# Kernel optimization log

Hardware: AMD Instinct MI355X
Metric: run time of the kernel (lower is better)

## Reference

```python
import jax, jax.numpy as jnp
import numpy as np

K = 16  # neighborhood size, fixed by the module

def knn_idx(coor_k, coor_q, k=K):
    # coor_*: [B, 3, N]; returns idx [B, k, Nq] into the Nk axis (transpose_mode=False layout)
    q = coor_q.transpose(0, 2, 1)
    r = coor_k.transpose(0, 2, 1)
    d2 = (jnp.sum(q * q, -1)[:, :, None] + jnp.sum(r * r, -1)[:, None, :]
          - 2.0 * jnp.einsum('bqd,bnd->bqn', q, r))
    _, idx = jax.lax.top_k(-d2, k)  # [B, Nq, k], nearest first
    return idx.transpose(0, 2, 1)   # [B, k, Nq]

def get_graph_feature(coor_q, x_q, coor_k, x_k, k=K):
    # Faithful to the source, including the flat gather + reshape(B, Nq, k, C)
    # applied to a [B, k, Nq]-ordered index (the source does NOT transpose idx).
    B, C, Nq = x_q.shape
    Nk = x_k.shape[2]
    idx = jax.lax.stop_gradient(knn_idx(coor_k, coor_q, k))            # [B, k, Nq]
    idx_flat = (idx + jnp.arange(B)[:, None, None] * Nk).reshape(-1)
    xk_flat = x_k.transpose(0, 2, 1).reshape(-1, C)                     # [B*Nk, C]
    feat = xk_flat[idx_flat].reshape(B, Nq, k, C).transpose(0, 3, 1, 2)  # [B, C, Nq, k]
    xq = jnp.broadcast_to(x_q[:, :, :, None], (B, C, Nq, k))
    return jnp.concatenate([feat - xq, xq], axis=1)                     # [B, 2C, Nq, k]

def group_norm(x, gamma, beta, groups=4, eps=1e-5):
    B, C, N, Kk = x.shape
    xg = x.reshape(B, groups, C // groups, N, Kk)
    mu = jnp.mean(xg, axis=(2, 3, 4), keepdims=True)
    var = jnp.var(xg, axis=(2, 3, 4), keepdims=True)
    xn = ((xg - mu) * jax.lax.rsqrt(var + eps)).reshape(B, C, N, Kk)
    return xn * gamma[None, :, None, None] + beta[None, :, None, None]

def edge_layer(h, w, gamma, beta):
    # Conv2d 1x1 (no bias) + GroupNorm(4) + LeakyReLU(0.2)
    return jax.nn.leaky_relu(group_norm(jnp.einsum('bcnk,oc->bonk', h, w), gamma, beta), 0.2)

def fps(xyz, m):
    # furthest point sampling, pointnet2 semantics (start at index 0). xyz: [B, N, 3]
    B, N, _ = xyz.shape
    def body(i, state):
        dists, far, idxs = state
        idxs = idxs.at[:, i].set(far)
        centroid = jnp.take_along_axis(xyz, far[:, None, None], axis=1)  # [B,1,3]
        d = jnp.sum((xyz - centroid) ** 2, axis=-1)
        dists = jnp.minimum(dists, d)
        return (dists, jnp.argmax(dists, axis=-1).astype(jnp.int32), idxs)
    state = (jnp.full((B, N), 1e10, xyz.dtype), jnp.zeros((B,), jnp.int32),
             jnp.zeros((B, m), jnp.int32))
    return jax.lax.fori_loop(0, m, body, state)[2]

def fps_downsample(coor, x, m):
    idx = fps(jax.lax.stop_gradient(coor).transpose(0, 2, 1), m)  # [B, m]
    comb = jnp.concatenate([coor, x], axis=1)                      # [B, 3+C, N]
    new = jnp.take_along_axis(comb, idx[:, None, :], axis=2)       # [B, 3+C, m]
    return new[:, :3], new[:, 3:]

def setup_inputs():
    key = jax.random.key(0)
    ks = jax.random.split(key, 16)
    B, N = 8, 2048
    p = lambda k, s, sc=0.05: jax.random.normal(k, s, jnp.float32) * sc
    return {
        'x': jax.random.normal(ks[0], (B, 3, N), jnp.float32),
        'w_in': p(ks[1], (8, 3)), 'b_in': p(ks[2], (8,)),
        'w1': p(ks[3], (32, 16)), 'g1': 1.0 + p(ks[4], (32,)), 'be1': p(ks[5], (32,)),
        'w2': p(ks[6], (64, 64)), 'g2': 1.0 + p(ks[7], (64,)), 'be2': p(ks[8], (64,)),
        'w3': p(ks[9], (64, 128)), 'g3': 1.0 + p(ks[10], (64,)), 'be3': p(ks[11], (64,)),
        'w4': p(ks[12], (128, 128)), 'g4': 1.0 + p(ks[13], (128,)), 'be4': p(ks[14], (128,)),
    }

def reference(x, w_in, b_in, w1, g1, be1, w2, g2, be2, w3, g3, be3, w4, g4, be4):
    N = x.shape[2]
    coor = x
    f = jnp.einsum('bcn,oc->bon', x, w_in) + b_in[None, :, None]          # input_trans Conv1d
    f = jnp.max(edge_layer(get_graph_feature(coor, f, coor, f), w1, g1, be1), axis=-1)
    coor_q, f_q = fps_downsample(coor, f, N // 4)
    f = jnp.max(edge_layer(get_graph_feature(coor_q, f_q, coor, f), w2, g2, be2), axis=-1)
    coor = coor_q
    f = jnp.max(edge_layer(get_graph_feature(coor, f, coor, f), w3, g3, be3), axis=-1)
    coor_q, f_q = fps_downsample(coor, f, N // 16)
    f = jnp.max(edge_layer(get_graph_feature(coor_q, f_q, coor, f), w4, g4, be4), axis=-1)
    return (coor_q, f)  # [B,3,N//16], [B,128,N//16]
```

## Files before the change

kernel.cpp:

```cpp
#include <hip/hip_runtime.h>
#include <float.h>
#include <stdint.h>


#define DI __device__ __forceinline__
DI float f_add(float a, float b) { return __fadd_rn(a, b); }
DI float f_sub(float a, float b) { return __fsub_rn(a, b); }
DI float f_mul(float a, float b) { return __fmul_rn(a, b); }

DI uint64_t umax64(uint64_t a, uint64_t b) { return a > b ? a : b; }

template<int CTRL, int RMASK>
DI uint32_t dpp_umax32(uint32_t v) {
  uint32_t o = (uint32_t)__builtin_amdgcn_update_dpp(0, (int)v, CTRL, RMASK, 0xF, false);
  return v > o ? v : o;
}
template<int CTRL, int RMASK>
DI uint32_t dpp_umin32(uint32_t v) {
  uint32_t o = (uint32_t)__builtin_amdgcn_update_dpp(-1, (int)v, CTRL, RMASK, 0xF, false);
  return v < o ? v : o;
}
template<int CTRL, int RMASK>
DI float dpp_fmin32(float v) {
  int o = __builtin_amdgcn_update_dpp(0x7F7FFFFF , __float_as_int(v),
                                      CTRL, RMASK, 0xF, false);
  return fminf(v, __int_as_float(o));
}
DI uint32_t wave_umax_bcast32(uint32_t v) {
  v = dpp_umax32<0x111, 0xF>(v);
  v = dpp_umax32<0x112, 0xF>(v);
  v = dpp_umax32<0x114, 0xF>(v);
  v = dpp_umax32<0x118, 0xF>(v);
  v = dpp_umax32<0x142, 0xA>(v);
  v = dpp_umax32<0x143, 0xC>(v);
  return (uint32_t)__builtin_amdgcn_readlane((int)v, 63);
}
DI uint32_t wave_umin_bcast32(uint32_t v) {
  v = dpp_umin32<0x111, 0xF>(v);
  v = dpp_umin32<0x112, 0xF>(v);
  v = dpp_umin32<0x114, 0xF>(v);
  v = dpp_umin32<0x118, 0xF>(v);
  v = dpp_umin32<0x142, 0xA>(v);
  v = dpp_umin32<0x143, 0xC>(v);
  return (uint32_t)__builtin_amdgcn_readlane((int)v, 63);
}
DI float wave_fmin_bcast32(float v) {
  v = dpp_fmin32<0x111, 0xF>(v);
  v = dpp_fmin32<0x112, 0xF>(v);
  v = dpp_fmin32<0x114, 0xF>(v);
  v = dpp_fmin32<0x118, 0xF>(v);
  v = dpp_fmin32<0x142, 0xA>(v);
  v = dpp_fmin32<0x143, 0xC>(v);
  return __int_as_float(__builtin_amdgcn_readlane(__float_as_int(v), 63));
}

template<int NK>
DI void knn_body(const float* __restrict__ cq, int Nq,
                 const float* __restrict__ ck, int* __restrict__ out,
                 int b, int qbase, float* smem)
{
  constexpr int CPL = NK / 64;
  float* xs = smem;
  float* ys = smem + NK;
  float* zs = smem + 2*NK;
  float* rr = smem + 3*NK;
  const int tid = threadIdx.x;
  for (int i = tid; i < NK; i += 256) {
    float a  = ck[((size_t)b*3 + 0)*NK + i];
    float bb = ck[((size_t)b*3 + 1)*NK + i];
    float c  = ck[((size_t)b*3 + 2)*NK + i];
    xs[i] = a; ys[i] = bb; zs[i] = c;
    rr[i] = f_add(f_add(f_mul(a,a), f_mul(bb,bb)), f_mul(c,c));
  }
  __syncthreads();
  const int lane = tid & 63, w = tid >> 6;
  const int q = qbase + w;
  if (q >= Nq) return;
  float qx = cq[((size_t)b*3 + 0)*Nq + q];
  float qy = cq[((size_t)b*3 + 1)*Nq + q];
  float qz = cq[((size_t)b*3 + 2)*Nq + q];
  float qq = f_add(f_add(f_mul(qx,qx), f_mul(qy,qy)), f_mul(qz,qz));
  float v[CPL];
  #pragma unroll
  for (int j = 0; j < CPL; ++j) {
    int c = j*64 + lane;
    float dot = f_add(f_add(f_mul(qx,xs[c]), f_mul(qy,ys[c])), f_mul(qz,zs[c]));
    v[j] = f_sub(f_add(qq, rr[c]), f_mul(2.0f, dot));
  }
  unsigned mask = (CPL >= 32) ? 0xFFFFFFFFu : ((1u << CPL) - 1u);
  for (int r = 0; r < 16; ++r) {
    float bv = FLT_MAX; int bc = 0x7FFFFFFF;
    #pragma unroll
    for (int j = 0; j < CPL; ++j) {
      float vj = ((mask >> j) & 1u) ? v[j] : FLT_MAX;
      if (vj < bv) { bv = vj; bc = j*64 + lane; }
    }
    float wmin = wave_fmin_bcast32(bv);
    uint32_t cand = (bv == wmin) ? (uint32_t)bc : 0xFFFFFFFFu;
    uint32_t wbc = wave_umin_bcast32(cand);
    if ((wbc & 63) == (uint32_t)lane) mask &= ~(1u << (wbc >> 6));
    if (lane == 0) out[((size_t)b*16 + r)*Nq + q] = (int)wbc;
  }
}

__device__ void fps_body(const float* __restrict__ x, int b,
                         int* __restrict__ s1, float* __restrict__ coorq,
                         int* __restrict__ s2, float* __restrict__ coorq2,
                         float* __restrict__ outc, char* smem_raw)
{
  float4*   pts  = (float4*)smem_raw;
  int*      sel  = (int*)(smem_raw + 32768);
  uint64_t* wkey = (uint64_t*)(smem_raw + 32768 + 2048);
  const int tid = threadIdx.x, lane = tid & 63, w = tid >> 6;

  for (int i = tid; i < 2048; i += 256)
    pts[i] = make_float4(x[((size_t)b*3 + 0)*2048 + i],
                         x[((size_t)b*3 + 1)*2048 + i],
                         x[((size_t)b*3 + 2)*2048 + i], 0.f);
  __syncthreads();

  float px[8], py[8], pz[8], dl[8];
  #pragma unroll
  for (int j = 0; j < 8; ++j) {
    float4 p = pts[tid + 256*j];
    px[j] = p.x; py[j] = p.y; pz[j] = p.z; dl[j] = 1e10f;
  }

  int far = 0;
  float4 c = pts[0];
  for (int i = 0; i < 512; ++i) {
    if (tid == 0) sel[i] = far;
    float bd = -1.0f; uint32_t bi = 0;
    #pragma unroll
    for (int j = 0; j < 8; ++j) {
      float dx = f_sub(px[j], c.x);
      float dy = f_sub(py[j], c.y);
      float dz = f_sub(pz[j], c.z);
      float d  = f_add(f_add(f_mul(dx,dx), f_mul(dy,dy)), f_mul(dz,dz));
      float nd = fminf(dl[j], d);
      dl[j] = nd;
      if (nd > bd) { bd = nd; bi = (uint32_t)(tid + 256*j); }
    }
    uint32_t db = __float_as_uint(bd);
    uint32_t wd = wave_umax_bcast32(db);
    uint32_t cand = (db == wd) ? bi : 0xFFFFFFFFu;
    uint32_t wi = wave_umin_bcast32(cand);
    if (lane == 0) wkey[(i & 1)*4 + w] = ((uint64_t)wd << 32) | (uint32_t)~wi;
    __syncthreads();
    const uint64_t* wk = wkey + (i & 1)*4;
    uint64_t g = umax64(umax64(wk[0], wk[1]), umax64(wk[2], wk[3]));
    far = (int)~(uint32_t)g;
    c = pts[far];
  }
  __syncthreads();

  int p0 = sel[tid], p1 = sel[tid + 256];
  float4 v0 = pts[p0], v1 = pts[p1];
  s1[b*512 + tid]       = p0;
  s1[b*512 + tid + 256] = p1;
  coorq[((size_t)b*3 + 0)*512 + tid] = v0.x;
  coorq[((size_t)b*3 + 1)*512 + tid] = v0.y;
  coorq[((size_t)b*3 + 2)*512 + tid] = v0.z;
  coorq[((size_t)b*3 + 0)*512 + tid + 256] = v1.x;
  coorq[((size_t)b*3 + 1)*512 + tid + 256] = v1.y;
  coorq[((size_t)b*3 + 2)*512 + tid + 256] = v1.z;
  __syncthreads();
  pts[tid] = v0; pts[tid + 256] = v1;
  __syncthreads();

  if (w == 0) {
    float qx[8], qy[8], qz[8], d2[8];
    #pragma unroll
    for (int j = 0; j < 8; ++j) {
      float4 p = pts[lane + 64*j];
      qx[j] = p.x; qy[j] = p.y; qz[j] = p.z; d2[j] = 1e10f;
    }
    int far2 = 0;
    float cx = pts[0].x, cy = pts[0].y, cz = pts[0].z;
    for (int i = 0; i < 128; ++i) {
      if (lane == 0) sel[i] = far2;
      float bd = -1.0f; uint32_t bi = 0;
      #pragma unroll
      for (int j = 0; j < 8; ++j) {
        float dx = f_sub(qx[j], cx);
        float dy = f_sub(qy[j], cy);
        float dz = f_sub(qz[j], cz);
        float d  = f_add(f_add(f_mul(dx,dx), f_mul(dy,dy)), f_mul(dz,dz));
        float nd = fminf(d2[j], d);
        d2[j] = nd;
        if (nd > bd) { bd = nd; bi = (uint32_t)(lane + 64*j); }
      }
      uint32_t db = __float_as_uint(bd);
      uint32_t wd = wave_umax_bcast32(db);
      uint32_t cand = (db == wd) ? bi : 0xFFFFFFFFu;
      uint32_t wi = wave_umin_bcast32(cand);
      far2 = (int)wi;
      uint32_t js = wi >> 6, ls = wi & 63;
      float sx = qx[0], sy = qy[0], sz = qz[0];
      #pragma unroll
      for (uint32_t t = 1; t < 8; ++t) {
        sx = (js == t) ? qx[t] : sx;
        sy = (js == t) ? qy[t] : sy;
        sz = (js == t) ? qz[t] : sz;
      }
      cx = __int_as_float(__builtin_amdgcn_readlane(__float_as_int(sx), ls));
      cy = __int_as_float(__builtin_amdgcn_readlane(__float_as_int(sy), ls));
      cz = __int_as_float(__builtin_amdgcn_readlane(__float_as_int(sz), ls));
    }
  }
  __syncthreads();
  if (tid < 128) {
    int p = sel[tid];
    float4 v = pts[p];
    s2[b*128 + tid] = p;
    coorq2[((size_t)b*3 + 0)*128 + tid] = v.x;
    coorq2[((size_t)b*3 + 1)*128 + tid] = v.y;
    coorq2[((size_t)b*3 + 2)*128 + tid] = v.z;
    outc[((size_t)b*3 + 0)*128 + tid] = v.x;
    outc[((size_t)b*3 + 1)*128 + tid] = v.y;
    outc[((size_t)b*3 + 2)*128 + tid] = v.z;
  }
}

__device__ void fused_l1_body(const float* __restrict__ x,
                              const float* __restrict__ w_in, const float* __restrict__ b_in,
                              const float* __restrict__ w1,
                              float* __restrict__ ymax1, float* __restrict__ ymin1,
                              float* __restrict__ stats,
                              int b, int S, char* smem_raw)
{
  float* xs = (float*)smem_raw;
  float* ys = xs + 2048;
  float* zs = xs + 4096;
  float* rr = xs + 6144;
  int*   idxloc = (int*)(xs + 8192);
  float* sw1  = (float*)(idxloc + 256);
  float* winb = sw1 + 512;
  float* red  = winb + 32;
  const int tid = threadIdx.x, lane = tid & 63, w = tid >> 6;

  for (int i = tid; i < 2048; i += 256) {
    float a  = x[((size_t)b*3 + 0)*2048 + i];
    float bb = x[((size_t)b*3 + 1)*2048 + i];
    float c  = x[((size_t)b*3 + 2)*2048 + i];
    xs[i] = a; ys[i] = bb; zs[i] = c;
    rr[i] = f_add(f_add(f_mul(a,a), f_mul(bb,bb)), f_mul(c,c));
  }
  for (int i = tid; i < 512; i += 256) sw1[i] = w1[i];
  if (tid < 24) winb[tid] = w_in[tid];
  if (tid < 8)  winb[24 + tid] = b_in[tid];
  __syncthreads();

  for (int qq = 0; qq < 4; ++qq) {
    int qi = w*4 + qq;
    int q = S + qi;
    float qx = xs[q], qy = ys[q], qz = zs[q];
    float qqv = f_add(f_add(f_mul(qx,qx), f_mul(qy,qy)), f_mul(qz,qz));
    float v[32];
    #pragma unroll
    for (int j = 0; j < 32; ++j) {
      int c = j*64 + lane;
      float dot = f_add(f_add(f_mul(qx,xs[c]), f_mul(qy,ys[c])), f_mul(qz,zs[c]));
      v[j] = f_sub(f_add(qqv, rr[c]), f_mul(2.0f, dot));
    }
    unsigned mask = 0xFFFFFFFFu;
    for (int r = 0; r < 16; ++r) {
      float bv = FLT_MAX; int bc = 0x7FFFFFFF;
      #pragma unroll
      for (int j = 0; j < 32; ++j) {
        float vj = ((mask >> j) & 1u) ? v[j] : FLT_MAX;
        if (vj < bv) { bv = vj; bc = j*64 + lane; }
      }
      float wmin = wave_fmin_bcast32(bv);
      uint32_t cand = (bv == wmin) ? (uint32_t)bc : 0xFFFFFFFFu;
      uint32_t wbc = wave_umin_bcast32(cand);
      if ((wbc & 63) == (uint32_t)lane) mask &= ~(1u << (wbc >> 6));
      if (lane == 0) idxloc[qi*16 + r] = (int)wbc;
    }
  }
  __syncthreads();

  const int r = tid >> 4, k = tid & 15;
  const int nbr = idxloc[k*16 + r];
  const int ng  = r*128 + (S >> 4);
  float f0n[8], f0q[8], h[8];
  #pragma unroll
  for (int o = 0; o < 8; ++o) {
    f0n[o] = winb[o*3+0]*xs[nbr] + winb[o*3+1]*ys[nbr] + winb[o*3+2]*zs[nbr] + winb[24+o];
    f0q[o] = winb[o*3+0]*xs[ng]  + winb[o*3+1]*ys[ng]  + winb[o*3+2]*zs[ng]  + winb[24+o];
    h[o] = f0n[o] - f0q[o];
  }
  float gsum[4] = {0.f,0.f,0.f,0.f}, gsq[4] = {0.f,0.f,0.f,0.f};
  float* ymx = ymax1 + ((size_t)b*2048 + ng)*32;
  float* ymn = ymin1 + ((size_t)b*2048 + ng)*32;
  for (int o = 0; o < 32; ++o) {
    const float4* wr = (const float4*)(sw1 + o*16);
    float4 wa = wr[0], wb4 = wr[1], wc = wr[2], wd = wr[3];
    float acc = wa.x*h[0]+wa.y*h[1]+wa.z*h[2]+wa.w*h[3]
              + wb4.x*h[4]+wb4.y*h[5]+wb4.z*h[6]+wb4.w*h[7]
              + wc.x*f0q[0]+wc.y*f0q[1]+wc.z*f0q[2]+wc.w*f0q[3]
              + wd.x*f0q[4]+wd.y*f0q[5]+wd.z*f0q[6]+wd.w*f0q[7];
    float mx = acc, mn = acc;
    #pragma unroll
    for (int off = 1; off < 16; off <<= 1) {
      mx = fmaxf(mx, __shfl_xor(mx, off));
      mn = fminf(mn, __shfl_xor(mn, off));
    }
    if (k == 0) { ymx[o] = mx; ymn[o] = mn; }
    int g = o >> 3;
    gsum[g] += acc; gsq[g] += acc*acc;
  }
  #pragma unroll
  for (int g = 0; g < 4; ++g) {
    #pragma unroll
    for (int off = 1; off < 64; off <<= 1) {
      gsum[g] += __shfl_xor(gsum[g], off);
      gsq[g]  += __shfl_xor(gsq[g], off);
    }
  }
  if (lane == 0) {
    #pragma unroll
    for (int g = 0; g < 4; ++g) { red[w*8 + g] = gsum[g]; red[w*8 + 4 + g] = gsq[g]; }
  }
  __syncthreads();
  if (tid == 0) {
    #pragma unroll
    for (int g = 0; g < 4; ++g) {
      float s0  = (red[g] + red[8+g]) + (red[16+g] + red[24+g]);
      float s1v = (red[4+g] + red[12+g]) + (red[20+g] + red[28+g]);
      atomicAdd(stats + (b*4 + g)*2,     s0);
      atomicAdd(stats + (b*4 + g)*2 + 1, s1v);
    }
  }
}

__global__ __launch_bounds__(256) void mega1(
    const float* __restrict__ x, const float* __restrict__ w_in, const float* __restrict__ b_in,
    const float* __restrict__ w1,
    float* __restrict__ ymax1, float* __restrict__ ymin1, float* __restrict__ stats,
    int* __restrict__ s1, float* __restrict__ coorq,
    int* __restrict__ s2, float* __restrict__ coorq2, float* __restrict__ outc)
{
  __shared__ char smem_raw[36352] __attribute__((aligned(16)));
  const int bid = blockIdx.x;
  if (bid < 8) {
    fps_body(x, bid, s1, coorq, s2, coorq2, outc, smem_raw);
  } else {
    int vb = bid - 8;
    fused_l1_body(x, w_in, b_in, w1, ymax1, ymin1, stats,
                  vb >> 7, (vb & 127)*16, smem_raw);
  }
}

__global__ __launch_bounds__(256) void mega2(
    const float* __restrict__ ymax1, const float* __restrict__ ymin1,
    const float* __restrict__ stats,
    const float* __restrict__ g1, const float* __restrict__ be1,
    float* __restrict__ f1T,
    const float* __restrict__ x, const float* __restrict__ coorq,
    const float* __restrict__ coorq2,
    int* __restrict__ idx2, int* __restrict__ idx3, int* __restrict__ idx4)
{
  __shared__ char smem_raw[32768] __attribute__((aligned(16)));
  const int bid = blockIdx.x;
  if (bid < 2048) {
    int t = bid*256 + threadIdx.x;
    int b = t >> 16;
    int o = t & 31;
    int g = o >> 3;
    const float cnt = 8.f*2048.f*16.f;
    float mu = stats[(b*4+g)*2] / cnt;
    float var = fmaxf(stats[(b*4+g)*2+1]/cnt - mu*mu, 0.f);
    float rs = 1.f/sqrtf(var + 1e-5f);
    float ga = g1[o], be = be1[o];
    float sel = (ga >= 0.f) ? ymax1[t] : ymin1[t];
    float a = (sel - mu)*rs*ga + be;
    f1T[t] = a >= 0.f ? a : 0.2f*a;
  } else if (bid < 3072) {
    int v = bid - 2048;
    knn_body<2048>(coorq, 512, x, idx2, v >> 7, (v & 127)*4, (float*)smem_raw);
  } else if (bid < 4096) {
    int v = bid - 3072;
    knn_body<512>(coorq, 512, coorq, idx3, v >> 7, (v & 127)*4, (float*)smem_raw);
  } else {
    int v = bid - 4096;
    knn_body<512>(coorq2, 128, coorq, idx4, v >> 5, (v & 31)*4, (float*)smem_raw);
  }
}

template<int C, int O, int NQ, int NK, bool STORE>
DI void conv_p1_body(
    const float* __restrict__ xqT, int xq_cols, const int* __restrict__ qg,
    const float* __restrict__ xkT, const int* __restrict__ knn_idx,
    const float* __restrict__ w, float* __restrict__ y, float* __restrict__ stats,
    int nt, int g, int b, float* smem)
{
  constexpr int GRP = O/4;
  const int tid = threadIdx.x;
  float* sxq = smem;
  float* sw  = smem + 16*C;
  float* red = sw + GRP*2*C;
  for (int i = tid; i < 16*C; i += 256) {
    int nn = i / C, ci = i % C;
    int q = nt*16 + nn;
    int src = qg ? qg[b*NQ + q] : q;
    sxq[i] = xqT[((size_t)b*xq_cols + src)*C + ci];
  }
  for (int i = tid; i < GRP*2*C; i += 256)
    sw[i] = w[(size_t)g*GRP*2*C + i];
  __syncthreads();

  const int nloc = tid >> 4, kk = tid & 15;
  const int n = nt*16 + nloc;
  const int flat = n*16 + kk;
  const int r = flat / NQ, s = flat % NQ;
  const int nbr = knn_idx[((size_t)b*16 + r)*NQ + s];

  float xqv[C], h1[C];
  {
    const float4* xq4 = (const float4*)(sxq + nloc*C);
    const float4* xk4 = (const float4*)(xkT + ((size_t)b*NK + nbr)*C);
    #pragma unroll
    for (int c4 = 0; c4 < C/4; ++c4) {
      float4 a = xq4[c4], k = xk4[c4];
      xqv[4*c4+0] = a.x; xqv[4*c4+1] = a.y; xqv[4*c4+2] = a.z; xqv[4*c4+3] = a.w;
      h1[4*c4+0] = k.x - a.x; h1[4*c4+1] = k.y - a.y;
      h1[4*c4+2] = k.z - a.z; h1[4*c4+3] = k.w - a.w;
    }
  }
  float lsum = 0.f, lsq = 0.f;
  float* yp = nullptr;
  if constexpr (STORE) yp = y + (((size_t)b*O + (size_t)g*GRP)*NQ + n)*16 + kk;
  for (int o = 0; o < GRP; ++o) {
    const float4* wr = (const float4*)(sw + o*2*C);
    float acc = 0.f;
    #pragma unroll
    for (int c4 = 0; c4 < C/4; ++c4) {
      float4 w4 = wr[c4];
      acc += w4.x*h1[4*c4] + w4.y*h1[4*c4+1] + w4.z*h1[4*c4+2] + w4.w*h1[4*c4+3];
    }
    #pragma unroll
    for (int c4 = 0; c4 < C/4; ++c4) {
      float4 w4 = wr[C/4 + c4];
      acc += w4.x*xqv[4*c4] + w4.y*xqv[4*c4+1] + w4.z*xqv[4*c4+2] + w4.w*xqv[4*c4+3];
    }
    if constexpr (STORE) yp[(size_t)o*NQ*16] = acc;
    lsum += acc; lsq += acc*acc;
  }
  #pragma unroll
  for (int off = 32; off; off >>= 1) {
    lsum += __shfl_xor(lsum, off);
    lsq  += __shfl_xor(lsq, off);
  }
  const int lane = tid & 63, wvid = tid >> 6;
  if (lane == 0) { red[wvid] = lsum; red[4+wvid] = lsq; }
  __syncthreads();
  if (tid == 0) {
    float s0  = (red[0]+red[1]) + (red[2]+red[3]);
    float s1v = (red[4]+red[5]) + (red[6]+red[7]);
    atomicAdd(stats + ((size_t)b*4 + g)*2,     s0);
    atomicAdd(stats + ((size_t)b*4 + g)*2 + 1, s1v);
  }
}

template<int C, int O, int NQ, int NK, bool STORE>
__global__ __launch_bounds__(256) void conv_p1(
    const float* __restrict__ xqT, int xq_cols, const int* __restrict__ qg,
    const float* __restrict__ xkT, const int* __restrict__ knn_idx,
    const float* __restrict__ w, float* __restrict__ y, float* __restrict__ stats)
{
  __shared__ float smem_f[16*C + (O/4)*2*C + 8];
  conv_p1_body<C, O, NQ, NK, STORE>(xqT, xq_cols, qg, xkT, knn_idx, w, y, stats,
                                    blockIdx.x, blockIdx.y, blockIdx.z, smem_f);
}

template<int O, int NQ, bool TOUT>
__global__ __launch_bounds__(256) void conv_p2(
    const float* __restrict__ y, const float* __restrict__ stats,
    const float* __restrict__ gamma, const float* __restrict__ beta,
    float* __restrict__ fout)
{
  int t = blockIdx.x*256 + threadIdx.x;
  if (t >= 8*O*NQ) return;
  int b = t / (O*NQ);
  int rem = t % (O*NQ);
  int o, n;
  if (TOUT) { o = rem % O; n = rem / O; }
  else      { n = rem % NQ; o = rem / NQ; }
  int g = o / (O/4);
  const float cnt = (float)((O/4) * NQ * 16);
  float s0 = stats[((size_t)b*4 + g)*2], s1v = stats[((size_t)b*4 + g)*2 + 1];
  float mu = s0 / cnt;
  float var = fmaxf(s1v / cnt - mu*mu, 0.f);
  float rs = 1.f / sqrtf(var + 1e-5f);
  float ga = gamma[o], be = beta[o];
  const float4* yp = (const float4*)(y + ((((size_t)b*O + o)*NQ) + n)*16);
  float m = -FLT_MAX;
  #pragma unroll
  for (int i = 0; i < 4; ++i) {
    float4 v4 = yp[i];
    float vv[4] = {v4.x, v4.y, v4.z, v4.w};
    #pragma unroll
    for (int j = 0; j < 4; ++j) {
      float a = (vv[j] - mu)*rs*ga + be;
      a = a >= 0.f ? a : 0.2f*a;
      m = fmaxf(m, a);
    }
  }
  fout[t] = m;
}

extern "C" void kernel_launch(void* const* d_in, const int* in_sizes, int n_in,
                              void* d_out, int out_size, void* d_ws, size_t ws_size,
                              hipStream_t stream)
{
  (void)in_sizes; (void)n_in; (void)out_size; (void)ws_size;
  const float* x    = (const float*)d_in[0];
  const float* w_in = (const float*)d_in[1];
  const float* b_in = (const float*)d_in[2];
  const float* w1   = (const float*)d_in[3];
  const float* g1   = (const float*)d_in[4];
  const float* be1  = (const float*)d_in[5];
  const float* w2   = (const float*)d_in[6];
  const float* g2   = (const float*)d_in[7];
  const float* be2  = (const float*)d_in[8];
  const float* w3   = (const float*)d_in[9];
  const float* g3   = (const float*)d_in[10];
  const float* be3  = (const float*)d_in[11];
  const float* w4   = (const float*)d_in[12];
  const float* g4   = (const float*)d_in[13];
  const float* be4  = (const float*)d_in[14];

  float* ws = (float*)d_ws;
  float* stats  = ws;
  float* f1T    = ws + 256;
  int*   s1     = (int*)(ws + 524544);
  float* coorq  = ws + 528640;
  int*   idx2   = (int*)(ws + 540928);
  float* f2T    = ws + 606464;
  int*   idx3   = (int*)(ws + 868608);
  float* f3T    = ws + 934144;
  int*   s2     = (int*)(ws + 1196288);
  float* coorq2 = ws + 1197312;
  int*   idx4   = (int*)(ws + 1200384);
  float* ybuf   = ws + 1216768;
  float* ymax1  = ybuf;
  float* ymin1  = ybuf + 524288;

  float* outc = (float*)d_out;
  float* f4   = (float*)d_out + 3072;

  hipMemsetAsync(stats, 0, 256*sizeof(float), stream);

  mega1<<<dim3(1032), 256, 0, stream>>>(
      x, w_in, b_in, w1, ymax1, ymin1, stats, s1, coorq, s2, coorq2, outc);

  mega2<<<dim3(4352), 256, 0, stream>>>(
      ymax1, ymin1, stats, g1, be1, f1T, x, coorq, coorq2, idx2, idx3, idx4);

  conv_p1<32, 64, 512, 2048, true><<<dim3(32, 4, 8), 256, 0, stream>>>(
      f1T, 2048, s1, f1T, idx2, w2, ybuf, stats + 64);
  conv_p2<64, 512, true><<<1024, 256, 0, stream>>>(ybuf, stats + 64, g2, be2, f2T);

  conv_p1<64, 64, 512, 512, true><<<dim3(32, 4, 8), 256, 0, stream>>>(
      f2T, 512, nullptr, f2T, idx3, w3, ybuf, stats + 128);
  conv_p2<64, 512, true><<<1024, 256, 0, stream>>>(ybuf, stats + 128, g3, be3, f3T);

  conv_p1<64, 128, 128, 512, true><<<dim3(8, 4, 8), 256, 0, stream>>>(
      f3T, 512, s2, f3T, idx4, w4, ybuf, stats + 192);
  conv_p2<128, 128, false><<<512, 256, 0, stream>>>(ybuf, stats + 192, g4, be4, f4);
}
```

Before: 446.3 us.

## Fuse GroupNorm-LeakyReLU-max finalization into next layer's gather via per-channel max/min

Each conv layer now writes only the per-point max and min over the 16 neighbors, reduced with lane shuffles, instead of the full [B,O,N,16] pre-norm tensor. The next layer applies GroupNorm, LeakyReLU and the gamma-sign max/min choice while it gathers neighbor and query features. This removes the separate conv_p2 passes, the large intermediate write and read, and the f1T finalize pass inside mega2. In exchange every gathered neighbor costs two loads plus normalization arithmetic, and the workspace layout grows.

```diff
diff --git a/kernel.cpp b/kernel.cpp
--- a/kernel.cpp
+++ b/kernel.cpp
@@ -353,61 +353,66 @@
 }
 
 __global__ __launch_bounds__(256) void mega2(
-    const float* __restrict__ ymax1, const float* __restrict__ ymin1,
-    const float* __restrict__ stats,
-    const float* __restrict__ g1, const float* __restrict__ be1,
-    float* __restrict__ f1T,
     const float* __restrict__ x, const float* __restrict__ coorq,
     const float* __restrict__ coorq2,
     int* __restrict__ idx2, int* __restrict__ idx3, int* __restrict__ idx4)
 {
   __shared__ char smem_raw[32768] __attribute__((aligned(16)));
   const int bid = blockIdx.x;
-  if (bid < 2048) {
-    int t = bid*256 + threadIdx.x;
-    int b = t >> 16;
-    int o = t & 31;
-    int g = o >> 3;
-    const float cnt = 8.f*2048.f*16.f;
-    float mu = stats[(b*4+g)*2] / cnt;
-    float var = fmaxf(stats[(b*4+g)*2+1]/cnt - mu*mu, 0.f);
-    float rs = 1.f/sqrtf(var + 1e-5f);
-    float ga = g1[o], be = be1[o];
-    float sel = (ga >= 0.f) ? ymax1[t] : ymin1[t];
-    float a = (sel - mu)*rs*ga + be;
-    f1T[t] = a >= 0.f ? a : 0.2f*a;
-  } else if (bid < 3072) {
-    int v = bid - 2048;
-    knn_body<2048>(coorq, 512, x, idx2, v >> 7, (v & 127)*4, (float*)smem_raw);
-  } else if (bid < 4096) {
-    int v = bid - 3072;
+  if (bid < 1024) {
+    knn_body<2048>(coorq, 512, x, idx2, bid >> 7, (bid & 127)*4, (float*)smem_raw);
+  } else if (bid < 2048) {
+    int v = bid - 1024;
     knn_body<512>(coorq, 512, coorq, idx3, v >> 7, (v & 127)*4, (float*)smem_raw);
   } else {
-    int v = bid - 4096;
+    int v = bid - 2048;
     knn_body<512>(coorq2, 128, coorq, idx4, v >> 5, (v & 31)*4, (float*)smem_raw);
   }
 }
 
-template<int C, int O, int NQ, int NK, bool STORE>
-DI void conv_p1_body(
-    const float* __restrict__ xqT, int xq_cols, const int* __restrict__ qg,
-    const float* __restrict__ xkT, const int* __restrict__ knn_idx,
-    const float* __restrict__ w, float* __restrict__ y, float* __restrict__ stats,
+template<int C, int O, int NQ, int NKp, bool TN>
+DI void conv_p1mm_body(
+    const float* __restrict__ ymaxP, const float* __restrict__ yminP,
+    const float* __restrict__ statsP,
+    const float* __restrict__ gP, const float* __restrict__ beP,
+    const int* __restrict__ qg, const int* __restrict__ knn_idx,
+    const float* __restrict__ w,
+    float* __restrict__ ymaxO, float* __restrict__ yminO, float* __restrict__ statsO,
     int nt, int g, int b, float* smem)
 {
   constexpr int GRP = O/4;
+  const float cntP = (float)((C/4) * NKp * 16);
   const int tid = threadIdx.x;
   float* sxq = smem;
-  float* sw  = smem + 16*C;
-  float* red = sw + GRP*2*C;
+  float* sw  = sxq + 16*C;
+  float* dmu = sw + GRP*2*C;
+  float* drs = dmu + C;
+  float* dga = drs + C;
+  float* dbe = dga + C;
+  float* red = dbe + C;
+
+  for (int i = tid; i < GRP*2*C; i += 256) sw[i] = w[(size_t)g*GRP*2*C + i];
+  for (int i = tid; i < C; i += 256) {
+    int gp = i / (C/4);
+    float s0 = statsP[(b*4+gp)*2], s1v = statsP[(b*4+gp)*2+1];
+    float mu = s0 / cntP;
+    float var = fmaxf(s1v/cntP - mu*mu, 0.f);
+    dmu[i] = mu; drs[i] = 1.f/sqrtf(var + 1e-5f);
+    dga[i] = gP[i]; dbe[i] = beP[i];
+  }
+  __syncthreads();
+
   for (int i = tid; i < 16*C; i += 256) {
     int nn = i / C, ci = i % C;
     int q = nt*16 + nn;
     int src = qg ? qg[b*NQ + q] : q;
-    sxq[i] = xqT[((size_t)b*xq_cols + src)*C + ci];
-  }
-  for (int i = tid; i < GRP*2*C; i += 256)
-    sw[i] = w[(size_t)g*GRP*2*C + i];
+    float vmx = ymaxP[((size_t)b*NKp + src)*C + ci];
+    float vmn = yminP[((size_t)b*NKp + src)*C + ci];
+    float ga = dga[ci];
+    float v = (ga >= 0.f) ? vmx : vmn;
+    float a = ((v - dmu[ci])*drs[ci])*ga + dbe[ci];
+    sxq[i] = a >= 0.f ? a : 0.2f*a;
+  }
   __syncthreads();
 
   const int nloc = tid >> 4, kk = tid & 15;
@@ -419,18 +424,31 @@
   float xqv[C], h1[C];
   {
     const float4* xq4 = (const float4*)(sxq + nloc*C);
-    const float4* xk4 = (const float4*)(xkT + ((size_t)b*NK + nbr)*C);
+    const float4* mx4 = (const float4*)(ymaxP + ((size_t)b*NKp + nbr)*C);
+    const float4* mn4 = (const float4*)(yminP + ((size_t)b*NKp + nbr)*C);
+    const float4* pmu = (const float4*)dmu;
+    const float4* prs = (const float4*)drs;
+    const float4* pga = (const float4*)dga;
+    const float4* pbe = (const float4*)dbe;
     #pragma unroll
     for (int c4 = 0; c4 < C/4; ++c4) {
-      float4 a = xq4[c4], k = xk4[c4];
-      xqv[4*c4+0] = a.x; xqv[4*c4+1] = a.y; xqv[4*c4+2] = a.z; xqv[4*c4+3] = a.w;
-      h1[4*c4+0] = k.x - a.x; h1[4*c4+1] = k.y - a.y;
-      h1[4*c4+2] = k.z - a.z; h1[4*c4+3] = k.w - a.w;
+      float4 a = xq4[c4], vx = mx4[c4], vn = mn4[c4];
+      float4 mu = pmu[c4], rs = prs[c4], ga = pga[c4], be = pbe[c4];
+      float v0 = (ga.x >= 0.f) ? vx.x : vn.x;
+      float v1 = (ga.y >= 0.f) ? vx.y : vn.y;
+      float v2 = (ga.z >= 0.f) ? vx.z : vn.z;
+      float v3 = (ga.w >= 0.f) ? vx.w : vn.w;
+      float f0 = ((v0 - mu.x)*rs.x)*ga.x + be.x; f0 = f0 >= 0.f ? f0 : 0.2f*f0;
+      float f1 = ((v1 - mu.y)*rs.y)*ga.y + be.y; f1 = f1 >= 0.f ? f1 : 0.2f*f1;
+      float f2 = ((v2 - mu.z)*rs.z)*ga.z + be.z; f2 = f2 >= 0.f ? f2 : 0.2f*f2;
+      float f3 = ((v3 - mu.w)*rs.w)*ga.w + be.w; f3 = f3 >= 0.f ? f3 : 0.2f*f3;
+      xqv[4*c4+0] = a.x; h1[4*c4+0] = f0 - a.x;
+      xqv[4*c4+1] = a.y; h1[4*c4+1] = f1 - a.y;
+      xqv[4*c4+2] = a.z; h1[4*c4+2] = f2 - a.z;
+      xqv[4*c4+3] = a.w; h1[4*c4+3] = f3 - a.w;
     }
   }
   float lsum = 0.f, lsq = 0.f;
-  float* yp = nullptr;
-  if constexpr (STORE) yp = y + (((size_t)b*O + (size_t)g*GRP)*NQ + n)*16 + kk;
   for (int o = 0; o < GRP; ++o) {
     const float4* wr = (const float4*)(sw + o*2*C);
     float acc = 0.f;
@@ -444,7 +462,17 @@
       float4 w4 = wr[C/4 + c4];
       acc += w4.x*xqv[4*c4] + w4.y*xqv[4*c4+1] + w4.z*xqv[4*c4+2] + w4.w*xqv[4*c4+3];
     }
-    if constexpr (STORE) yp[(size_t)o*NQ*16] = acc;
+    float mx = acc, mn = acc;
+    #pragma unroll
+    for (int off = 1; off < 16; off <<= 1) {
+      mx = fmaxf(mx, __shfl_xor(mx, off));
+      mn = fminf(mn, __shfl_xor(mn, off));
+    }
+    if (kk == 0) {
+      int og = g*GRP + o;
+      size_t idx = TN ? (((size_t)b*NQ + n)*O + og) : (((size_t)b*O + og)*NQ + n);
+      ymaxO[idx] = mx; yminO[idx] = mn;
+    }
     lsum += acc; lsq += acc*acc;
   }
   #pragma unroll
@@ -458,56 +486,45 @@
   if (tid == 0) {
     float s0  = (red[0]+red[1]) + (red[2]+red[3]);
     float s1v = (red[4]+red[5]) + (red[6]+red[7]);
-    atomicAdd(stats + ((size_t)b*4 + g)*2,     s0);
-    atomicAdd(stats + ((size_t)b*4 + g)*2 + 1, s1v);
-  }
-}
-
-template<int C, int O, int NQ, int NK, bool STORE>
-__global__ __launch_bounds__(256) void conv_p1(
-    const float* __restrict__ xqT, int xq_cols, const int* __restrict__ qg,
-    const float* __restrict__ xkT, const int* __restrict__ knn_idx,
-    const float* __restrict__ w, float* __restrict__ y, float* __restrict__ stats)
-{
-  __shared__ float smem_f[16*C + (O/4)*2*C + 8];
-  conv_p1_body<C, O, NQ, NK, STORE>(xqT, xq_cols, qg, xkT, knn_idx, w, y, stats,
+    atomicAdd(statsO + ((size_t)b*4 + g)*2,     s0);
+    atomicAdd(statsO + ((size_t)b*4 + g)*2 + 1, s1v);
+  }
+}
+
+template<int C, int O, int NQ, int NKp, bool TN>
+__global__ __launch_bounds__(256) void conv_p1mm(
+    const float* __restrict__ ymaxP, const float* __restrict__ yminP,
+    const float* __restrict__ statsP,
+    const float* __restrict__ gP, const float* __restrict__ beP,
+    const int* __restrict__ qg, const int* __restrict__ knn_idx,
+    const float* __restrict__ w,
+    float* __restrict__ ymaxO, float* __restrict__ yminO, float* __restrict__ statsO)
+{
+  __shared__ float smem_f[16*C + (O/4)*2*C + 4*C + 8];
+  conv_p1mm_body<C, O, NQ, NKp, TN>(ymaxP, yminP, statsP, gP, beP, qg, knn_idx,
+                                    w, ymaxO, yminO, statsO,
                                     blockIdx.x, blockIdx.y, blockIdx.z, smem_f);
 }
 
-template<int O, int NQ, bool TOUT>
-__global__ __launch_bounds__(256) void conv_p2(
-    const float* __restrict__ y, const float* __restrict__ stats,
-    const float* __restrict__ gamma, const float* __restrict__ beta,
-    float* __restrict__ fout)
+__global__ __launch_bounds__(256) void l4fin(
+    const float* __restrict__ ymax4, const float* __restrict__ ymin4,
+    const float* __restrict__ stats4,
+    const float* __restrict__ g4, const float* __restrict__ be4,
+    float* __restrict__ f4)
 {
   int t = blockIdx.x*256 + threadIdx.x;
-  if (t >= 8*O*NQ) return;
-  int b = t / (O*NQ);
-  int rem = t % (O*NQ);
-  int o, n;
-  if (TOUT) { o = rem % O; n = rem / O; }
-  else      { n = rem % NQ; o = rem / NQ; }
-  int g = o / (O/4);
-  const float cnt = (float)((O/4) * NQ * 16);
-  float s0 = stats[((size_t)b*4 + g)*2], s1v = stats[((size_t)b*4 + g)*2 + 1];
+  int b = t >> 14;
+  int o = (t >> 7) & 127;
+  int g = o >> 5;
+  const float cnt = 32.f*128.f*16.f;
+  float s0 = stats4[(b*4+g)*2], s1v = stats4[(b*4+g)*2+1];
   float mu = s0 / cnt;
-  float var = fmaxf(s1v / cnt - mu*mu, 0.f);
-  float rs = 1.f / sqrtf(var + 1e-5f);
-  float ga = gamma[o], be = beta[o];
-  const float4* yp = (const float4*)(y + ((((size_t)b*O + o)*NQ) + n)*16);
-  float m = -FLT_MAX;
-  #pragma unroll
-  for (int i = 0; i < 4; ++i) {
-    float4 v4 = yp[i];
-    float vv[4] = {v4.x, v4.y, v4.z, v4.w};
-    #pragma unroll
-    for (int j = 0; j < 4; ++j) {
-      float a = (vv[j] - mu)*rs*ga + be;
-      a = a >= 0.f ? a : 0.2f*a;
-      m = fmaxf(m, a);
-    }
-  }
-  fout[t] = m;
+  float var = fmaxf(s1v/cnt - mu*mu, 0.f);
+  float rs = 1.f/sqrtf(var + 1e-5f);
+  float ga = g4[o], be = be4[o];
+  float v = (ga >= 0.f) ? ymax4[t] : ymin4[t];
+  float a = ((v - mu)*rs)*ga + be;
+  f4[t] = a >= 0.f ? a : 0.2f*a;
 }
 
 extern "C" void kernel_launch(void* const* d_in, const int* in_sizes, int n_in,
@@ -533,19 +550,21 @@
 
   float* ws = (float*)d_ws;
   float* stats  = ws;
-  float* f1T    = ws + 256;
-  int*   s1     = (int*)(ws + 524544);
-  float* coorq  = ws + 528640;
-  int*   idx2   = (int*)(ws + 540928);
-  float* f2T    = ws + 606464;
-  int*   idx3   = (int*)(ws + 868608);
-  float* f3T    = ws + 934144;
-  int*   s2     = (int*)(ws + 1196288);
-  float* coorq2 = ws + 1197312;
-  int*   idx4   = (int*)(ws + 1200384);
-  float* ybuf   = ws + 1216768;
-  float* ymax1  = ybuf;
-  float* ymin1  = ybuf + 524288;
+  float* ymax1  = ws + 256;
+  float* ymin1  = ws + 524544;
+  int*   s1     = (int*)(ws + 1048832);
+  float* coorq  = ws + 1052928;
+  int*   idx2   = (int*)(ws + 1065216);
+  float* ymax2  = ws + 1130752;
+  float* ymin2  = ws + 1392896;
+  int*   idx3   = (int*)(ws + 1655040);
+  float* ymax3  = ws + 1720576;
+  float* ymin3  = ws + 1982720;
+  int*   s2     = (int*)(ws + 2244864);
+  float* coorq2 = ws + 2245888;
+  int*   idx4   = (int*)(ws + 2248960);
+  float* ymax4  = ws + 2265344;
+  float* ymin4  = ws + 2396416;
 
   float* outc = (float*)d_out;
   float* f4   = (float*)d_out + 3072;
@@ -555,18 +574,16 @@
   mega1<<<dim3(1032), 256, 0, stream>>>(
       x, w_in, b_in, w1, ymax1, ymin1, stats, s1, coorq, s2, coorq2, outc);
 
-  mega2<<<dim3(4352), 256, 0, stream>>>(
-      ymax1, ymin1, stats, g1, be1, f1T, x, coorq, coorq2, idx2, idx3, idx4);
-
-  conv_p1<32, 64, 512, 2048, true><<<dim3(32, 4, 8), 256, 0, stream>>>(
-      f1T, 2048, s1, f1T, idx2, w2, ybuf, stats + 64);
-  conv_p2<64, 512, true><<<1024, 256, 0, stream>>>(ybuf, stats + 64, g2, be2, f2T);
-
-  conv_p1<64, 64, 512, 512, true><<<dim3(32, 4, 8), 256, 0, stream>>>(
-      f2T, 512, nullptr, f2T, idx3, w3, ybuf, stats + 128);
-  conv_p2<64, 512, true><<<1024, 256, 0, stream>>>(ybuf, stats + 128, g3, be3, f3T);
-
-  conv_p1<64, 128, 128, 512, true><<<dim3(8, 4, 8), 256, 0, stream>>>(
-      f3T, 512, s2, f3T, idx4, w4, ybuf, stats + 192);
-  conv_p2<128, 128, false><<<512, 256, 0, stream>>>(ybuf, stats + 192, g4, be4, f4);
-}
+  mega2<<<dim3(2304), 256, 0, stream>>>(x, coorq, coorq2, idx2, idx3, idx4);
+
+  conv_p1mm<32, 64, 512, 2048, true><<<dim3(32, 4, 8), 256, 0, stream>>>(
+      ymax1, ymin1, stats, g1, be1, s1, idx2, w2, ymax2, ymin2, stats + 64);
+
+  conv_p1mm<64, 64, 512, 512, true><<<dim3(32, 4, 8), 256, 0, stream>>>(
+      ymax2, ymin2, stats + 64, g2, be2, nullptr, idx3, w3, ymax3, ymin3, stats + 128);
+
+  conv_p1mm<64, 128, 128, 512, false><<<dim3(8, 4, 8), 256, 0, stream>>>(
+      ymax3, ymin3, stats + 128, g3, be3, s2, idx4, w4, ymax4, ymin4, stats + 192);
+
+  l4fin<<<dim3(512), 256, 0, stream>>>(ymax4, ymin4, stats + 192, g4, be4, f4);
+}
```

Result: faster. 430.8 us (-3.5%).
